# Kernel optimization log

Hardware: AMD Instinct MI355X
Metric: run time of the kernel (lower is better)

Reference implementation:

```python
import jax, jax.numpy as jnp
import numpy as np

B, N = 32, 1000
HID, COM = 256, 64
T_LEN, NOP = 288, 3
NVAL, TP_D, CS_D, TIME_D = 9, 2, 4, 4
IN_C = CS_D + TP_D + NVAL            # 15, competition GAT input
IN_CO = IN_C + COM                    # 79, cooperation GAT input
OBS = TIME_D + TP_D + CS_D + 2 * COM + NVAL  # 147
K_D = K_F = 500                       # int(0.5*N + 0.5)
TEMP = 1.0
NEG = jnp.float32(-1e8)


def setup_inputs() -> dict:
    key = jax.random.key(0)
    ks = jax.random.split(key, 24)
    def nrm(k, shp, scale=0.05):
        return (jax.random.normal(k, shp, dtype=jnp.float32) * scale)
    return {
        "time_idx": jax.random.randint(ks[0], (B, N), 0, T_LEN, dtype=jnp.int32),
        "op_idx": jax.random.randint(ks[1], (B, N), 0, NOP, dtype=jnp.int32),
        "value_feats": jax.random.normal(ks[2], (B, N, NVAL), dtype=jnp.float32),
        "dpcs_mark": jax.random.randint(ks[3], (B, N, 1), 0, 2) > 0,
        "adj_comp": jax.random.randint(ks[4], (B, N, N), 0, 2) > 0,
        "adj_coop": jax.random.randint(ks[5], (B, N, N), 0, 2) > 0,
        "distance": jax.random.uniform(ks[6], (N, N), dtype=jnp.float32),
        "time_tab": jax.random.uniform(ks[7], (T_LEN, TIME_D), dtype=jnp.float32),
        "tp_tab": jax.random.uniform(ks[8], (NOP, TP_D), dtype=jnp.float32),
        "cs_tab": jax.random.uniform(ks[9], (N, CS_D), dtype=jnp.float32),
        "Wc": nrm(ks[10], (IN_C, COM)),
        "asrc_c": nrm(ks[11], (COM,)),
        "adst_c": nrm(ks[12], (COM,)),
        "wd_c": jnp.float32(0.1),
        "Wco": nrm(ks[13], (IN_CO, COM)),
        "asrc_co": nrm(ks[14], (COM,)),
        "adst_co": nrm(ks[15], (COM,)),
        "wd_co": jnp.float32(0.1),
        "Wp": nrm(ks[16], (OBS, HID)),
        "bp": jnp.zeros((HID,), dtype=jnp.float32),
        "vpd": nrm(ks[17], (HID,)),
        "vpf": nrm(ks[18], (HID,)),
    }


def gat(x, W, a_src, a_dst, w_d, adj, dist):
    """Single-head GAT over dense boolean adjacency. adj[b,j,i] True => edge j->i."""
    h = jnp.einsum("bnf,fd->bnd", x, W)                       # (B,N,D)
    e = (jnp.einsum("bid,d->bi", h, a_dst)[:, :, None]        # dst term
         + jnp.einsum("bjd,d->bj", h, a_src)[:, None, :]      # src term
         + w_d * dist.T[None])                                 # dist[j,i] edge feat
    e = jax.nn.leaky_relu(e, 0.2)
    mask = jnp.swapaxes(adj, 1, 2)                             # (B, dst i, src j)
    e = jnp.where(mask, e, NEG)
    alpha = jax.nn.softmax(e, axis=-1)
    alpha = jnp.where(mask, alpha, 0.0)                        # isolated nodes -> 0
    return jax.nn.elu(jnp.einsum("bij,bjd->bid", alpha, h))


def gated_pool(x_p, scores, valid, k, temp):
    scores = scores - scores.max(axis=1, keepdims=True)
    scores = jnp.where(valid, scores, NEG)                     # (B,N,1)
    val_topk = jax.lax.top_k(scores[..., 0], k)[0]             # (B,k)
    min_topk = val_topk.min(axis=-1)[:, None, None]
    scores = jnp.where(scores < min_topk, NEG, scores)
    w = jax.nn.softmax(scores / temp, axis=1)
    xg = x_p * w
    return jnp.concatenate([xg.sum(axis=1), xg.max(axis=1)], axis=-1)  # (B,2H)


def reference(time_idx, op_idx, value_feats, dpcs_mark, adj_comp, adj_coop,
              distance, time_tab, tp_tab, cs_tab, Wc, asrc_c, adst_c, wd_c,
              Wco, asrc_co, adst_co, wd_co, Wp, bp, vpd, vpf):
    time_e = time_tab[time_idx]                                # (B,N,4)
    tp_e = tp_tab[op_idx]                                      # (B,N,2)
    cs_e = jnp.broadcast_to(cs_tab[None], (B, N, CS_D))        # (B,N,4)
    vf_det = jax.lax.stop_gradient(value_feats)
    x = jnp.concatenate([cs_e, tp_e, vf_det], axis=-1)         # (B,N,15)
    comp_reps = gat(x, Wc, asrc_c, adst_c, wd_c, adj_comp, distance)
    x_m = jnp.concatenate([x, comp_reps], axis=-1)             # (B,N,79)
    coop_reps = gat(x_m, Wco, asrc_co, adst_co, wd_co, adj_coop, distance)
    sag = jnp.concatenate([time_e, cs_e, tp_e, value_feats, comp_reps, coop_reps], axis=-1)
    x_p = jnp.einsum("bnf,fh->bnh", sag, Wp) + bp              # (B,N,HID)
    scores_d = jnp.einsum("bnh,h->bn", x_p, vpd)[..., None]
    s_d = gated_pool(x_p, scores_d, dpcs_mark, K_D, TEMP)
    scores_f = jnp.einsum("bnh,h->bn", x_p, vpf)[..., None]
    s_f = gated_pool(x_p, scores_f, ~dpcs_mark, K_F, TEMP)
    return jnp.concatenate([s_f, s_d], axis=-1)                # (B, 4*HID)
```

## Files before the change

### kernel.cpp

```cpp
#include <hip/hip_runtime.h>
#include <hip/hip_bf16.h>

#define NB 32
#define NN 1000
#define COMD 64
#define HIDD 256
#define KSEL 500
#define TI 16
#define GATX ((NN + TI - 1) / TI)
#define PACKX 32
#define NSPL 32
#define ROWS 32
#define DSTRIDE 1024

#define PB_AQ1  0
#define PB_DT   1024
#define PB_WP   1280
#define PB_WCO  1320
#define PB_MISC 1344
#define PB_EMB  1345
#define PB_N    (PB_EMB + NB * NN / 4)

typedef __hip_bfloat16 bf16;
typedef unsigned long long u64;
typedef __attribute__((ext_vector_type(4))) float f32x4;
typedef __attribute__((ext_vector_type(8))) short s16x8;
typedef __attribute__((ext_vector_type(4))) short s16x4;
typedef __attribute__((ext_vector_type(4))) unsigned short u16x4;
typedef __attribute__((ext_vector_type(2))) unsigned long long u64x2;

__device__ __forceinline__ float b2f(bf16 x){ return __bfloat162float(x); }

template<bool F32>
__device__ __forceinline__ float ldf(const void* p, long i){
  return F32 ? ((const float*)p)[i] : b2f(((const bf16*)p)[i]);
}
template<bool BINT>
__device__ __forceinline__ bool ldb(const void* p, long i){
  return BINT ? (((const int*)p)[i] != 0) : (((const unsigned char*)p)[i] != 0);
}

__device__ __forceinline__ float wave_sum(float v){
#pragma unroll
  for (int o = 32; o > 0; o >>= 1) v += __shfl_down(v, o, 64);
  return v;
}
__device__ __forceinline__ float wave_bsum(float v){
#pragma unroll
  for (int o = 32; o > 0; o >>= 1) v += __shfl_xor(v, o, 64);
  return v;
}
__device__ __forceinline__ float wave_bmax(float v){
#pragma unroll
  for (int o = 32; o > 0; o >>= 1) v = fmaxf(v, __shfl_xor(v, o, 64));
  return v;
}
__device__ __forceinline__ int wave_bsum_i(int v){
#pragma unroll
  for (int o = 32; o > 0; o >>= 1) v += __shfl_xor(v, o, 64);
  return v;
}
__device__ __forceinline__ unsigned fkey(float f){
// ... 184 lines not shown
  }
  ad = wave_bsum(ad); af = wave_bsum(af);
  if (lane == 0){ wv_ws[f] = ad; wv_ws[160 + f] = af; }
}
template<bool F32>
__device__ __forceinline__ void wco_role(const void* Wco, const void* asrc, const void* adst,
                         short* WcoB_hi, short* WcoB_lo, float* pvco, int rel){
  int t = threadIdx.x;
  int g = t >> 6, lane = t & 63;
  int f = rel * 4 + g;
  float w = (f < 79) ? ldf<F32>(Wco, (long)f * COMD + lane) : 0.f;
  int kb = f >> 5, q = (f >> 3) & 3, u = f & 7;
  long off = (((long)(kb * 4 + q)) * 64 + lane) * 8 + u;
  short hi, lo; split_bf(w, hi, lo);
  WcoB_hi[off] = hi; WcoB_lo[off] = lo;
  float dd = wave_bsum(w * ldf<F32>(adst, lane));
  float ss = wave_bsum(w * ldf<F32>(asrc, lane));
  if (lane == 0){ pvco[f] = dd; pvco[96 + f] = ss; }
}
template<bool F32>
__device__ __forceinline__ void misc_role(const void* wdc, const void* wdco,
                          const void* bp, const void* vpd, const void* vpf,
                          int f32, int as_int,
                          int* flags, float* wd_ws, float* wv_ws){
  int t = threadIdx.x;
  if (t >= 64) return;
  int lane = t;
  float ad = 0.f, af = 0.f;
#pragma unroll
  for (int r = 0; r < 4; ++r){
    int ch = r * 64 + lane;
    float bb = ldf<F32>(bp, ch);
    ad += bb * ldf<F32>(vpd, ch);
    af += bb * ldf<F32>(vpf, ch);
  }
  ad = wave_bsum(ad); af = wave_bsum(af);
  if (lane == 0){
    wv_ws[320] = ad; wv_ws[321] = af;
    wd_ws[0] = ldf<F32>(wdc, 0);
    wd_ws[1] = ldf<F32>(wdco, 0);
    flags[0] = f32; flags[1] = as_int;
  }
}
template<bool F32>
__device__ __forceinline__ void embed_body(
    const int* op_idx, const void* vf, const void* cs_tab, const void* tp_tab,
    const void* Wc, const void* asrc, const void* adst,
    float* x_out, short* hB_hi, short* hB_lo, float* ed_out, float* es_out,
    int rel){
  int t = threadIdx.x;
// ... 7 lines not shown
    float x_f;
    if (f < 4)      x_f = ldf<F32>(cs_tab, n * 4 + f);
    else if (f < 6) x_f = ldf<F32>(tp_tab, op * 2 + (f - 4));
    else            x_f = ldf<F32>(vf, (long)g * 9 + (f - 6));
    if (lane == f) xv = x_f;
    hacc += x_f * ldf<F32>(Wc, f * COMD + lane);
  }
  if (lane < 15) x_out[g * 15 + lane] = xv;
  hB_write(hB_hi, hB_lo, b, n, lane, hacc);
  float sd = wave_sum(hacc * ldf<F32>(adst, lane));
  float ss = wave_sum(hacc * ldf<F32>(asrc, lane));
  if (lane == 0){ ed_out[g] = sd; es_out[g] = ss; }
}
__global__ void __launch_bounds__(256) k_prep(
    const void* dist, const void* adj_comp,
    const void* wdc, const void* wdco,
    const void* Wp, const void* vpd, const void* vpf, const void* bp,
    const void* Wco, const void* asrc_co, const void* adst_co,
    const int* op_idx, const void* vfeat, const void* cs_tab, const void* tp_tab,
    const void* Wc, const void* asrc_c, const void* adst_c,
    int* flags, float* wd_ws, bf16* distTb, u64* adjQc,
    short* WpB_hi, short* WpB_lo, float* wv_ws,
    short* WcoB_hi, short* WcoB_lo, float* pvco,
    float* x_ws, short* hB_hi, short* hB_lo, float* ed_c, float* es_c){
  __shared__ __attribute__((aligned(16))) char smem[SMEM_BYTES];
  int blk = blockIdx.x;
  int f32, as_int;
  sniff2(dist, adj_comp, threadIdx.x & 63, f32, as_int);
  if (blk < PB_DT){
    if (as_int) adjq_role<true >(adj_comp, adjQc, blk - PB_AQ1, smem);
    else        adjq_role<false>(adj_comp, adjQc, blk - PB_AQ1, smem);
  } else if (blk < PB_WP){
    if (f32) dist_t_role<true >(dist, distTb, blk - PB_DT, smem);
    else     dist_t_role<false>(dist, distTb, blk - PB_DT, smem);
  } else if (blk < PB_WCO){
    if (f32) wp_role<true >(Wp, vpd, vpf, WpB_hi, WpB_lo, wv_ws, blk - PB_WP);
    else     wp_role<false>(Wp, vpd, vpf, WpB_hi, WpB_lo, wv_ws, blk - PB_WP);
  } else if (blk < PB_MISC){
    if (f32) wco_role<true >(Wco, asrc_co, adst_co, WcoB_hi, WcoB_lo, pvco, blk - PB_WCO);
    else     wco_role<false>(Wco, asrc_co, adst_co, WcoB_hi, WcoB_lo, pvco, blk - PB_WCO);
  } else if (blk < PB_EMB){
    if (f32) misc_role<true >(wdc, wdco, bp, vpd, vpf, f32, as_int, flags, wd_ws, wv_ws);
    else     misc_role<false>(wdc, wdco, bp, vpd, vpf, f32, as_int, flags, wd_ws, wv_ws);
  } else {
    if (f32) embed_body<true >(op_idx, vfeat, cs_tab, tp_tab, Wc, asrc_c, adst_c,
                               x_ws, hB_hi, hB_lo, ed_c, es_c, blk - PB_EMB);
    else     embed_body<false>(op_idx, vfeat, cs_tab, tp_tab, Wc, asrc_c, adst_c,
                               x_ws, hB_hi, hB_lo, ed_c, es_c, blk - PB_EMB);
  }
}

template<bool HCO>
__device__ __forceinline__ void gat_body(
    const float* __restrict__ ed, const float* __restrict__ es,
    const float* __restrict__ wd_ws, int wd_idx, const u64* __restrict__ adjQ,
    const bf16* __restrict__ distTb,
    const short* __restrict__ hB_hi, const short* __restrict__ hB_lo,
    float* __restrict__ reps,
    const int* __restrict__ flags, const void* adj_raw, u64* adjQ_out,
    const float* __restrict__ x_ws,
    const short* __restrict__ WcoB_hi, const short* __restrict__ WcoB_lo,
    const float* __restrict__ pvco,
    short* hB2_hi, short* hB2_lo, float* ed_o, float* es_o){
  __shared__ short pA[32 * 544] __attribute__((aligned(16)));
  __shared__ float redz[TI][4];
  __shared__ float esred[4];
  if (HCO && blockIdx.x >= GATX){
    int rel = (blockIdx.x - GATX) * NB + blockIdx.y;
    if (flags[1]) adjq_role<true >(adj_raw, adjQ_out, rel, (void*)pA);
    else          adjq_role<false>(adj_raw, adjQ_out, rel, (void*)pA);
    return;
  }
  int t = threadIdx.x;
  int wv = t >> 6, lane = t & 63;
  int b = blockIdx.y;
  int i0 = blockIdx.x * TI;
  float wd = wd_ws[wd_idx];
  int iw = i0 >> 6;
  int sb2 = (i0 & 63) >> 2;
  int j0 = t * 4;

  const u64* aq = adjQ + ((long)b * 16 + iw) * 1024 + j0;
  u64x2 wA = *(const u64x2*)&aq[0];
  u64x2 wB = *(const u64x2*)&aq[2];
  u64 wsh[4] = { wA[0] >> sb2, wA[1] >> sb2, wB[0] >> sb2, wB[1] >> sb2 };
  float4 es4 = *(const float4*)&es[(long)b * NN + j0];
  float esv[4] = {es4.x, es4.y, es4.z, es4.w};
  float esm = -1e30f;
#pragma unroll
  for (int c = 0; c < 4; ++c)
// ... 51 lines not shown
  int q = lane >> 4, m = lane & 15;
  int abase = q * 136 + m * 8;
  int ch = wv * 16 + m;
  const short* bh = hB_hi + (long)b * 65536 + ((long)q * 64 + ch) * 8;
  const short* bl = hB_lo + (long)b * 65536 + ((long)q * 64 + ch) * 8;
  f32x4 acc = {0.f, 0.f, 0.f, 0.f};
#pragma unroll
  for (int kb = 0; kb < 32; ++kb){
    s16x8 a   = *(const s16x8*)&pA[kb * 544 + abase];
    s16x8 bhi = *(const s16x8*)&bh[(long)kb * 2048];
    s16x8 blo = *(const s16x8*)&bl[(long)kb * 2048];
    acc = __builtin_amdgcn_mfma_f32_16x16x32_bf16(a, bhi, acc, 0, 0, 0);
    acc = __builtin_amdgcn_mfma_f32_16x16x32_bf16(a, blo, acc, 0, 0, 0);
  }
  float vr[4];
#pragma unroll
  for (int reg = 0; reg < 4; ++reg){
    int ti = (lane >> 4) * 4 + reg;
    float z = redz[ti][0] + redz[ti][1] + redz[ti][2] + redz[ti][3];
    float zi = (z > 0.f) ? 1.f / z : 0.f;
    float v = acc[reg] * zi;
    v = (v > 0.f) ? v : expm1f(v);
    vr[reg] = v;
    int ch2 = wv * 16 + (lane & 15);
    if (i0 + ti < NN)
      reps[((long)b * NN + i0 + ti) * COMD + ch2] = v;
  }
  if (!HCO) return;

  __syncthreads();
  float* cx = (float*)pA;
  short* cA_hi = pA + 2560;
  short* cA_lo = pA + 2560 + 1920;
  {
    int ch2 = wv * 16 + (lane & 15);
#pragma unroll
    for (int reg = 0; reg < 4; ++reg){
      int row = (lane >> 4) * 4 + reg;
      cx[row * 80 + 15 + ch2] = vr[reg];
    }
  }
  for (int idx = t; idx < 16 * 15; idx += 256){
    int nl = idx / 15, f = idx - nl * 15;
    int i = i0 + nl; int ic = (i < NN) ? i : (NN - 1);
    cx[nl * 80 + f] = x_ws[((long)b * NN + ic) * 15 + f];
  }
  __syncthreads();
  {
    int node = t >> 4, sub = t & 15;
    float dd = 0.f, ss = 0.f;
    for (int f = sub; f < 79; f += 16){
      float c = cx[node * 80 + f];
      dd += c * pvco[f];
      ss += c * pvco[96 + f];
    }
#pragma unroll
    for (int o = 8; o > 0; o >>= 1){
      dd += __shfl_xor(dd, o, 64);
      ss += __shfl_xor(ss, o, 64);
    }
    if (sub == 0 && i0 + node < NN){
      ed_o[(long)b * NN + i0 + node] = dd;
      es_o[(long)b * NN + i0 + node] = ss;
    }
  }
  for (int idx = t; idx < 16 * 96; idx += 256){
    int mm = idx / 96, k = idx - mm * 96;
    float v = (k < 79) ? cx[mm * 80 + k] : 0.f;
    int kb = k >> 5, qq = (k >> 3) & 3, u = k & 7;
    short hi, lo; split_bf(v, hi, lo);
    int off = (kb * 16 + mm) * 40 + qq * 8 + u;
    cA_hi[off] = hi; cA_lo[off] = lo;
  }
  __syncthreads();
  {
    int q2 = lane >> 4, m2 = lane & 15;
    int ch3 = wv * 16 + m2;
    f32x4 a2 = {0.f, 0.f, 0.f, 0.f};
#pragma unroll
    for (int kb = 0; kb < 3; ++kb){
      int aoff = (kb * 16 + m2) * 40 + q2 * 8;
      s16x8 a_hi = *(const s16x8*)&cA_hi[aoff];
      s16x8 a_lo = *(const s16x8*)&cA_lo[aoff];
      long boff = (((long)(kb * 4 + q2)) * 64 + ch3) * 8;
      s16x8 b_hi = *(const s16x8*)&WcoB_hi[boff];
      s16x8 b_lo = *(const s16x8*)&WcoB_lo[boff];
      a2 = __builtin_amdgcn_mfma_f32_16x16x32_bf16(a_hi, b_hi, a2, 0, 0, 0);
      a2 = __builtin_amdgcn_mfma_f32_16x16x32_bf16(a_hi, b_lo, a2, 0, 0, 0);
      a2 = __builtin_amdgcn_mfma_f32_16x16x32_bf16(a_lo, b_hi, a2, 0, 0, 0);
    }
#pragma unroll
    for (int reg = 0; reg < 4; ++reg){
      int row = (lane >> 4) * 4 + reg;
      int n2 = i0 + row;
      hB_write(hB2_hi, hB2_lo, b, n2, ch3, a2[reg]);
    }
  }
}
__global__ void __launch_bounds__(256) k_gat1(
    const float* ed, const float* es, const float* wd_ws, const u64* adjQ,
    const bf16* distTb, const short* hB_hi, const short* hB_lo, float* reps,
    const int* flags, const void* adj_raw, u64* adjQ_out,
    const float* x_ws, const short* WcoB_hi, const short* WcoB_lo,
    const float* pvco, short* hB2_hi, short* hB2_lo, float* ed_o, float* es_o){
  gat_body<true>(ed, es, wd_ws, 0, adjQ, distTb, hB_hi, hB_lo, reps,
                 flags, adj_raw, adjQ_out, x_ws, WcoB_hi, WcoB_lo, pvco,
                 hB2_hi, hB2_lo, ed_o, es_o);
}
__global__ void __launch_bounds__(256) k_gat2(
    const float* ed, const float* es, const float* wd_ws, const u64* adjQ,
    const bf16* distTb, const short* hB_hi, const short* hB_lo, float* reps){
  gat_body<false>(ed, es, wd_ws, 1, adjQ, distTb, hB_hi, hB_lo, reps,
                  nullptr, nullptr, nullptr, nullptr, nullptr, nullptr,
                  nullptr, nullptr, nullptr, nullptr, nullptr);
}

template<bool F32>
__device__ __forceinline__ void xp_body(
    const int* time_idx, const int* op_idx, const void* vf, const void* time_tab,
    const void* cs_tab, const void* tp_tab, const float* comp, const float* coop,
    const short* __restrict__ WpB_hi, const short* __restrict__ WpB_lo,
    const float* __restrict__ wv_ws, const void* bp,
    float* x_p, float* scf, float* scd){
  __shared__ float sagF[16][148] __attribute__((aligned(16)));
  __shared__ short sagA_hi[5 * 16 * 40] __attribute__((aligned(16)));
  __shared__ short sagA_lo[5 * 16 * 40] __attribute__((aligned(16)));
  int t = threadIdx.x;
  int wv = t >> 6, lane = t & 63;
  int base = blockIdx.x * 16;

  for (int idx = t; idx < 16 * 147; idx += 256){
    int nl = idx / 147, f = idx - nl * 147;
    int g = base + nl;
    int n = g % NN;
    float v;
    if (f < 4)       v = ldf<F32>(time_tab, time_idx[g] * 4 + f);
    else if (f < 8)  v = ldf<F32>(cs_tab, n * 4 + (f - 4));
    else if (f < 10) v = ldf<F32>(tp_tab, op_idx[g] * 2 + (f - 8));
    else if (f < 19) v = ldf<F32>(vf, (long)g * 9 + (f - 10));
    else if (f < 83) v = comp[(long)g * COMD + (f - 19)];
    else             v = coop[(long)g * COMD + (f - 83)];
    sagF[nl][f] = v;
  }
  __syncthreads();

  for (int idx = t; idx < 16 * 160; idx += 256){
    int m = idx / 160, k = idx - m * 160;
    float v = (k < 147) ? sagF[m][k] : 0.f;
    int kb = k >> 5, q = (k >> 3) & 3, u = k & 7;
    short hi, lo; split_bf(v, hi, lo);
    int off = (kb * 16 + m) * 40 + q * 8 + u;
    sagA_hi[off] = hi; sagA_lo[off] = lo;
  }
  {
    int node = t >> 4, sub = t & 15;
    float ad = 0.f, af = 0.f;
    for (int f = sub; f < 147; f += 16){
      float s = sagF[node][f];
      ad += s * wv_ws[f];
      af += s * wv_ws[160 + f];
    }
#pragma unroll
    for (int o = 8; o > 0; o >>= 1){
      ad += __shfl_xor(ad, o, 64);
      af += __shfl_xor(af, o, 64);
    }
    if (sub == 0){
      scd[base + node] = ad + wv_ws[320];
      scf[base + node] = af + wv_ws[321];
    }
  }
  __syncthreads();

  int Ag = lane >> 4, Am = lane & 15;
  f32x4 acc[4] = {{0,0,0,0},{0,0,0,0},{0,0,0,0},{0,0,0,0}};
#pragma unroll
  for (int kb = 0; kb < 5; ++kb){
    int aoff = (kb * 16 + Am) * 40 + Ag * 8;
    s16x8 a_hi = *(const s16x8*)&sagA_hi[aoff];
    s16x8 a_lo = *(const s16x8*)&sagA_lo[aoff];
#pragma unroll
    for (int ct = 0; ct < 4; ++ct){
      int ch = wv * 64 + ct * 16 + Am;
      long boff = (((long)(kb * 4 + Ag)) * 256 + ch) * 8;
      s16x8 b_hi = *(const s16x8*)&WpB_hi[boff];
      s16x8 b_lo = *(const s16x8*)&WpB_lo[boff];
      acc[ct] = __builtin_amdgcn_mfma_f32_16x16x32_bf16(a_hi, b_hi, acc[ct], 0, 0, 0);
      acc[ct] = __builtin_amdgcn_mfma_f32_16x16x32_bf16(a_hi, b_lo, acc[ct], 0, 0, 0);
      acc[ct] = __builtin_amdgcn_mfma_f32_16x16x32_bf16(a_lo, b_hi, acc[ct], 0, 0, 0);
    }
  }
#pragma unroll
  for (int ct = 0; ct < 4; ++ct){
    int ch = wv * 64 + ct * 16 + (lane & 15);
    float bb = ldf<F32>(bp, ch);
#pragma unroll
    for (int reg = 0; reg < 4; ++reg){
      int row = (lane >> 4) * 4 + reg;
      x_p[(long)(base + row) * HIDD + ch] = acc[ct][reg] + bb;
    }
  }
}
__global__ void __launch_bounds__(256) k_xp(
    const int* flags, const int* time_idx, const int* op_idx, const void* vf,
    const void* time_tab, const void* cs_tab, const void* tp_tab,
    const float* comp, const float* coop,
    const short* WpB_hi, const short* WpB_lo, const float* wv_ws, const void* bp,
    float* x_p, float* scf, float* scd){
  if (flags[0]) xp_body<true >(time_idx, op_idx, vf, time_tab, cs_tab, tp_tab, comp, coop, WpB_hi, WpB_lo, wv_ws, bp, x_p, scf, scd);
  else          xp_body<false>(time_idx, op_idx, vf, time_tab, cs_tab, tp_tab, comp, coop, WpB_hi, WpB_lo, wv_ws, bp, x_p, scf, scd);
}

template<bool BINT>
__device__ __forceinline__ void topk_body(
    const float* scf, const float* scd, const void* mark, float* wls){
  int lane = threadIdx.x;
  int b = blockIdx.x, pool = blockIdx.y;
  const float* sc = (pool == 0) ? scf : scd;
  float v[16]; unsigned key[16];
  float m0 = -INFINITY;
#pragma unroll
  for (int r = 0; r < 16; ++r){
    int n = r * 64 + lane;
    float s = (n < NN) ? sc[b * NN + n] : -INFINITY;
    v[r] = s;
    m0 = fmaxf(m0, s);
  }
  m0 = wave_bmax(m0);
  float m1 = -INFINITY;
#pragma unroll
  for (int r = 0; r < 16; ++r){
    int n = r * 64 + lane;
    bool valid = false;
    if (n < NN){
      bool mk = ldb<BINT>(mark, b * NN + n);
      valid = (pool == 0) ? !mk : mk;
    }
    v[r] = valid ? (v[r] - m0) : -1e8f;
    key[r] = fkey(v[r]);
    if (n < NN) m1 = fmaxf(m1, v[r]);
  }
  m1 = wave_bmax(m1);

  unsigned lo = 0u, hi = 0xFFFFFFFFu;
  while (lo < hi){
    unsigned mid = lo + ((hi - lo) >> 1) + 1u;
    int c = 0;
#pragma unroll
    for (int r = 0; r < 16; ++r) c += (key[r] >= mid) ? 1 : 0;
    c = wave_bsum_i(c);
    if (c >= KSEL) lo = mid; else hi = mid - 1u;
  }

  float p[16];
  float ls = 0.f;
#pragma unroll
  for (int r = 0; r < 16; ++r){
    int n = r * 64 + lane;
    float pp = (n < NN && key[r] >= lo) ? __expf(v[r] - m1) : 0.f;
    p[r] = pp;
    ls += pp;
  }
  ls = wave_bsum(ls);
  float zinv = (ls > 0.f) ? 1.f / ls : 0.f;
  float* w_out = wls + ((long)b * 2 + pool) * 1024;
#pragma unroll
  for (int r = 0; r < 16; ++r){
    int n = r * 64 + lane;
    if (n < NN) w_out[n] = p[r] * zinv;
  }
}
__global__ void k_topk(const int* flags, const float* scf, const float* scd,
                       const void* mark, float* wls){
  if (flags[1]) topk_body<true >(scf, scd, mark, wls);
  else          topk_body<false>(scf, scd, mark, wls);
}

__global__ void __launch_bounds__(256) k_psum(
    const float* __restrict__ wls, const float* __restrict__ x_p,
    float* __restrict__ part){
  __shared__ float wf[ROWS], wdd[ROWS];
  int t = threadIdx.x;
  int b = blockIdx.x, z = blockIdx.y;
  int n0 = z * ROWS;
  int ns = min(ROWS, NN - n0);
  if (t < ns){
    wf[t]  = wls[((long)b * 2 + 0) * 1024 + n0 + t];
    wdd[t] = wls[((long)b * 2 + 1) * 1024 + n0 + t];
  }
  __syncthreads();
  float sf = 0.f, mf = -INFINITY, sd = 0.f, md = -INFINITY;
  const float* xb = x_p + ((long)b * NN + n0) * HIDD + t;
  for (int k = 0; k < ns; ++k){
    float xv = xb[(long)k * HIDD];
    float gf = wf[k] * xv;
    float gd = wdd[k] * xv;
    sf += gf; mf = fmaxf(mf, gf);
    sd += gd; md = fmaxf(md, gd);
  }
  long pb = (((long)b * NSPL + z) * 4) * HIDD + t;
  part[pb + 0 * HIDD] = sf;
  part[pb + 1 * HIDD] = mf;
  part[pb + 2 * HIDD] = sd;
  part[pb + 3 * HIDD] = md;
}

template<bool F32>
__device__ __forceinline__ void pfin_body(const float* part, void* out){
  int t = threadIdx.x;
  int b = blockIdx.x;
  float sf = 0.f, mf = -INFINITY, sd = 0.f, md = -INFINITY;
#pragma unroll
  for (int z = 0; z < NSPL; ++z){
    long pb = (((long)b * NSPL + z) * 4) * HIDD + t;
    sf += part[pb + 0 * HIDD];
    mf = fmaxf(mf, part[pb + 1 * HIDD]);
    sd += part[pb + 2 * HIDD];
    md = fmaxf(md, part[pb + 3 * HIDD]);
  }
  long ob = (long)b * 1024;
  if (F32){
    ((float*)out)[ob + t] = sf;
    ((float*)out)[ob + 256 + t] = mf;
    ((float*)out)[ob + 512 + t] = sd;
    ((float*)out)[ob + 768 + t] = md;
  } else {
    ((bf16*)out)[ob + t] = __float2bfloat16(sf);
    ((bf16*)out)[ob + 256 + t] = __float2bfloat16(mf);
    ((bf16*)out)[ob + 512 + t] = __float2bfloat16(sd);
    ((bf16*)out)[ob + 768 + t] = __float2bfloat16(md);
  }
}
__global__ void k_pfin(const int* flags, const float* part, void* out){
  if (flags[0]) pfin_body<true >(part, out);
  else          pfin_body<false>(part, out);
}

extern "C" void kernel_launch(void* const* d_in, const int* in_sizes, int n_in,
                              void* d_out, int out_size, void* d_ws, size_t ws_size,
                              hipStream_t stream){
  const int*  time_idx = (const int*)d_in[0];
  const int*  op_idx   = (const int*)d_in[1];
  const void* vfeat    = d_in[2];
  const void* dpcs     = d_in[3];
  const void* adj_comp = d_in[4];
  const void* adj_coop = d_in[5];
  const void* dist     = d_in[6];
  const void* time_tab = d_in[7];
  const void* tp_tab   = d_in[8];
  const void* cs_tab   = d_in[9];
  const void* Wc       = d_in[10];
  const void* asrc_c   = d_in[11];
  const void* adst_c   = d_in[12];
  const void* wd_c     = d_in[13];
  const void* Wco      = d_in[14];
  const void* asrc_co  = d_in[15];
  const void* adst_co  = d_in[16];
  const void* wd_co    = d_in[17];
  const void* Wp       = d_in[18];
  const void* bp       = d_in[19];
  const void* vpd      = d_in[20];
  const void* vpf      = d_in[21];

  char* ws = (char*)d_ws;
  size_t o = 0;
  auto alloc = [&](size_t bytes)->char*{
    char* p = ws + o; o = (o + bytes + 255) & ~(size_t)255; return p;
  };
  int*   flags   = (int*)alloc(16);
  float* wd_ws   = (float*)alloc(8);
  bf16*  distTb  = (bf16*)alloc((size_t)NN * DSTRIDE * 2);
  u64*   adjQc   = (u64*)alloc((size_t)NB * 16 * 1024 * 8);
  u64*   adjQo   = (u64*)alloc((size_t)NB * 16 * 1024 * 8);
  float* x_ws    = (float*)alloc((size_t)NB * NN * 15 * 4);
  float* comp    = (float*)alloc((size_t)NB * NN * COMD * 4);
  float* coop    = (float*)alloc((size_t)NB * NN * COMD * 4);
  short* hB_hi   = (short*)alloc((size_t)NB * 65536 * 2);
  short* hB_lo   = (short*)alloc((size_t)NB * 65536 * 2);
  short* hB2_hi  = (short*)alloc((size_t)NB * 65536 * 2);
  short* hB2_lo  = (short*)alloc((size_t)NB * 65536 * 2);
  short* WpB_hi  = (short*)alloc((size_t)5 * 4 * 256 * 8 * 2);
  short* WpB_lo  = (short*)alloc((size_t)5 * 4 * 256 * 8 * 2);
  short* WcoB_hi = (short*)alloc((size_t)3 * 4 * 64 * 8 * 2);
  short* WcoB_lo = (short*)alloc((size_t)3 * 4 * 64 * 8 * 2);
  float* wv_ws   = (float*)alloc(322 * 4);
  float* pvco    = (float*)alloc(192 * 4);
  float* ed_c    = (float*)alloc((size_t)NB * NN * 4 + 256);
  float* es_c    = (float*)alloc((size_t)NB * NN * 4 + 256);
  float* ed_o    = (float*)alloc((size_t)NB * NN * 4 + 256);
  float* es_o    = (float*)alloc((size_t)NB * NN * 4 + 256);
  float* scf     = (float*)alloc((size_t)NB * NN * 4);
  float* scd     = (float*)alloc((size_t)NB * NN * 4);
  float* wls     = (float*)alloc((size_t)NB * 2 * 1024 * 4);
  float* part    = (float*)alloc((size_t)NB * NSPL * 4 * HIDD * 4);
  float* x_p     = (float*)alloc((size_t)NB * NN * HIDD * 4);

  k_prep<<<dim3(PB_N), dim3(256), 0, stream>>>(
      dist, adj_comp, wd_c, wd_co, Wp, vpd, vpf, bp,
      Wco, asrc_co, adst_co,
      op_idx, vfeat, cs_tab, tp_tab, Wc, asrc_c, adst_c,
      flags, wd_ws, distTb, adjQc, WpB_hi, WpB_lo, wv_ws,
      WcoB_hi, WcoB_lo, pvco,
      x_ws, hB_hi, hB_lo, ed_c, es_c);
  k_gat1<<<dim3(GATX + PACKX, NB), dim3(256), 0, stream>>>(
      ed_c, es_c, wd_ws, adjQc, distTb, hB_hi, hB_lo, comp,
      flags, adj_coop, adjQo,
      x_ws, WcoB_hi, WcoB_lo, pvco, hB2_hi, hB2_lo, ed_o, es_o);
  k_gat2<<<dim3(GATX, NB), dim3(256), 0, stream>>>(
      ed_o, es_o, wd_ws, adjQo, distTb, hB2_hi, hB2_lo, coop);
  k_xp<<<dim3(NB * NN / 16), dim3(256), 0, stream>>>(
      flags, time_idx, op_idx, vfeat, time_tab, cs_tab, tp_tab, comp, coop,
      WpB_hi, WpB_lo, wv_ws, bp, x_p, scf, scd);
  k_topk<<<dim3(NB, 2), dim3(64), 0, stream>>>(flags, scf, scd, dpcs, wls);
  k_psum<<<dim3(NB, NSPL), dim3(256), 0, stream>>>(wls, x_p, part);
  k_pfin<<<dim3(NB), dim3(256), 0, stream>>>(flags, part, d_out);
}
```

Baseline: 465.7 us.

## Fuse projection into second GAT and merge topk/psum/finalize into one pool kernel

The x_p projection (sag concat plus the Wp MFMA) now runs inside the second GAT kernel's epilogue, so coop reps are never written to or re-read from global memory. Top-k selection, the weighted partial sums and the final reduction are merged into one pool kernel that uses an atomic counter so the last block per batch finalizes. This removes three kernel launches and the coop and wls round trips. In exchange, every pool block recomputes the top-k threshold redundantly, and the counter reset depends on the prep kernel.

```diff
diff --git a/kernel.cpp b/kernel.cpp
--- a/kernel.cpp
+++ b/kernel.cpp
@@ -35,9 +35,8 @@
 __device__ __forceinline__ float ldf(const void* p, long i){
   return F32 ? ((const float*)p)[i] : b2f(((const bf16*)p)[i]);
 }
-template<bool BINT>
-__device__ __forceinline__ bool ldb(const void* p, long i){
-  return BINT ? (((const int*)p)[i] != 0) : (((const unsigned char*)p)[i] != 0);
+__device__ __forceinline__ float ldr(const void* p, long i, int f32){
+  return f32 ? ((const float*)p)[i] : b2f(((const bf16*)p)[i]);
 }
 
 __device__ __forceinline__ float wave_sum(float v){
@@ -268,10 +267,11 @@
 __device__ __forceinline__ void misc_role(const void* wdc, const void* wdco,
                           const void* bp, const void* vpd, const void* vpf,
                           int f32, int as_int,
-                          int* flags, float* wd_ws, float* wv_ws){
+                          int* flags, float* wd_ws, float* wv_ws, int* ctr){
   int t = threadIdx.x;
   if (t >= 64) return;
   int lane = t;
+  if (lane < NB) ctr[lane] = 0;
   float ad = 0.f, af = 0.f;
 #pragma unroll
   for (int r = 0; r < 4; ++r){
@@ -325,7 +325,8 @@
     int* flags, float* wd_ws, bf16* distTb, u64* adjQc,
     short* WpB_hi, short* WpB_lo, float* wv_ws,
     short* WcoB_hi, short* WcoB_lo, float* pvco,
-    float* x_ws, short* hB_hi, short* hB_lo, float* ed_c, float* es_c){
+    float* x_ws, short* hB_hi, short* hB_lo, float* ed_c, float* es_c,
+    int* ctr){
   __shared__ __attribute__((aligned(16))) char smem[SMEM_BYTES];
   int blk = blockIdx.x;
   int f32, as_int;
@@ -343,8 +344,8 @@
     if (f32) wco_role<true >(Wco, asrc_co, adst_co, WcoB_hi, WcoB_lo, pvco, blk - PB_WCO);
     else     wco_role<false>(Wco, asrc_co, adst_co, WcoB_hi, WcoB_lo, pvco, blk - PB_WCO);
   } else if (blk < PB_EMB){
-    if (f32) misc_role<true >(wdc, wdco, bp, vpd, vpf, f32, as_int, flags, wd_ws, wv_ws);
-    else     misc_role<false>(wdc, wdco, bp, vpd, vpf, f32, as_int, flags, wd_ws, wv_ws);
+    if (f32) misc_role<true >(wdc, wdco, bp, vpd, vpf, f32, as_int, flags, wd_ws, wv_ws, ctr);
+    else     misc_role<false>(wdc, wdco, bp, vpd, vpf, f32, as_int, flags, wd_ws, wv_ws, ctr);
   } else {
     if (f32) embed_body<true >(op_idx, vfeat, cs_tab, tp_tab, Wc, asrc_c, adst_c,
                                x_ws, hB_hi, hB_lo, ed_c, es_c, blk - PB_EMB);
@@ -353,7 +354,7 @@
   }
 }
 
-template<bool HCO>
+template<int MODE>
 __device__ __forceinline__ void gat_body(
     const float* __restrict__ ed, const float* __restrict__ es,
     const float* __restrict__ wd_ws, int wd_idx, const u64* __restrict__ adjQ,
@@ -364,11 +365,17 @@
     const float* __restrict__ x_ws,
     const short* __restrict__ WcoB_hi, const short* __restrict__ WcoB_lo,
     const float* __restrict__ pvco,
-    short* hB2_hi, short* hB2_lo, float* ed_o, float* es_o){
+    short* hB2_hi, short* hB2_lo, float* ed_o, float* es_o,
+    const int* __restrict__ time_idx, const int* __restrict__ op_idx,
+    const void* vf, const void* time_tab, const void* cs_tab, const void* tp_tab,
+    const float* __restrict__ comp,
+    const short* __restrict__ WpB_hi, const short* __restrict__ WpB_lo,
+    const float* __restrict__ wv_ws, const void* bp,
+    float* x_p, float* scf_o, float* scd_o){
   __shared__ short pA[32 * 544] __attribute__((aligned(16)));
   __shared__ float redz[TI][4];
   __shared__ float esred[4];
-  if (HCO && blockIdx.x >= GATX){
+  if (MODE == 0 && blockIdx.x >= GATX){
     int rel = (blockIdx.x - GATX) * NB + blockIdx.y;
     if (flags[1]) adjq_role<true >(adj_raw, adjQ_out, rel, (void*)pA);
     else          adjq_role<false>(adj_raw, adjQ_out, rel, (void*)pA);
@@ -466,78 +473,164 @@
     float v = acc[reg] * zi;
     v = (v > 0.f) ? v : expm1f(v);
     vr[reg] = v;
-    int ch2 = wv * 16 + (lane & 15);
-    if (i0 + ti < NN)
-      reps[((long)b * NN + i0 + ti) * COMD + ch2] = v;
-  }
-  if (!HCO) return;
-
-  __syncthreads();
-  float* cx = (float*)pA;
-  short* cA_hi = pA + 2560;
-  short* cA_lo = pA + 2560 + 1920;
-  {
-    int ch2 = wv * 16 + (lane & 15);
-#pragma unroll
-    for (int reg = 0; reg < 4; ++reg){
-      int row = (lane >> 4) * 4 + reg;
-      cx[row * 80 + 15 + ch2] = vr[reg];
-    }
-  }
-  for (int idx = t; idx < 16 * 15; idx += 256){
-    int nl = idx / 15, f = idx - nl * 15;
-    int i = i0 + nl; int ic = (i < NN) ? i : (NN - 1);
-    cx[nl * 80 + f] = x_ws[((long)b * NN + ic) * 15 + f];
-  }
-  __syncthreads();
-  {
-    int node = t >> 4, sub = t & 15;
-    float dd = 0.f, ss = 0.f;
-    for (int f = sub; f < 79; f += 16){
-      float c = cx[node * 80 + f];
-      dd += c * pvco[f];
-      ss += c * pvco[96 + f];
-    }
-#pragma unroll
-    for (int o = 8; o > 0; o >>= 1){
-      dd += __shfl_xor(dd, o, 64);
-      ss += __shfl_xor(ss, o, 64);
-    }
-    if (sub == 0 && i0 + node < NN){
-      ed_o[(long)b * NN + i0 + node] = dd;
-      es_o[(long)b * NN + i0 + node] = ss;
-    }
-  }
-  for (int idx = t; idx < 16 * 96; idx += 256){
-    int mm = idx / 96, k = idx - mm * 96;
-    float v = (k < 79) ? cx[mm * 80 + k] : 0.f;
-    int kb = k >> 5, qq = (k >> 3) & 3, u = k & 7;
-    short hi, lo; split_bf(v, hi, lo);
-    int off = (kb * 16 + mm) * 40 + qq * 8 + u;
-    cA_hi[off] = hi; cA_lo[off] = lo;
-  }
-  __syncthreads();
-  {
-    int q2 = lane >> 4, m2 = lane & 15;
-    int ch3 = wv * 16 + m2;
-    f32x4 a2 = {0.f, 0.f, 0.f, 0.f};
-#pragma unroll
-    for (int kb = 0; kb < 3; ++kb){
-      int aoff = (kb * 16 + m2) * 40 + q2 * 8;
-      s16x8 a_hi = *(const s16x8*)&cA_hi[aoff];
-      s16x8 a_lo = *(const s16x8*)&cA_lo[aoff];
-      long boff = (((long)(kb * 4 + q2)) * 64 + ch3) * 8;
-      s16x8 b_hi = *(const s16x8*)&WcoB_hi[boff];
-      s16x8 b_lo = *(const s16x8*)&WcoB_lo[boff];
-      a2 = __builtin_amdgcn_mfma_f32_16x16x32_bf16(a_hi, b_hi, a2, 0, 0, 0);
-      a2 = __builtin_amdgcn_mfma_f32_16x16x32_bf16(a_hi, b_lo, a2, 0, 0, 0);
-      a2 = __builtin_amdgcn_mfma_f32_16x16x32_bf16(a_lo, b_hi, a2, 0, 0, 0);
-    }
-#pragma unroll
-    for (int reg = 0; reg < 4; ++reg){
-      int row = (lane >> 4) * 4 + reg;
-      int n2 = i0 + row;
-      hB_write(hB2_hi, hB2_lo, b, n2, ch3, a2[reg]);
+    if (MODE == 0){
+      int ch2 = wv * 16 + (lane & 15);
+      if (i0 + ti < NN)
+        reps[((long)b * NN + i0 + ti) * COMD + ch2] = v;
+    }
+  }
+
+  if (MODE == 0){
+    __syncthreads();
+    float* cx = (float*)pA;
+    short* cA_hi = pA + 2560;
+    short* cA_lo = pA + 2560 + 1920;
+    {
+      int ch2 = wv * 16 + (lane & 15);
+#pragma unroll
+      for (int reg = 0; reg < 4; ++reg){
+        int row = (lane >> 4) * 4 + reg;
+        cx[row * 80 + 15 + ch2] = vr[reg];
+      }
+    }
+    for (int idx = t; idx < 16 * 15; idx += 256){
+      int nl = idx / 15, f = idx - nl * 15;
+      int i = i0 + nl; int ic = (i < NN) ? i : (NN - 1);
+      cx[nl * 80 + f] = x_ws[((long)b * NN + ic) * 15 + f];
+    }
+    __syncthreads();
+    {
+      int node = t >> 4, sub = t & 15;
+      float dd = 0.f, ss = 0.f;
+      for (int f = sub; f < 79; f += 16){
+        float c = cx[node * 80 + f];
+        dd += c * pvco[f];
+        ss += c * pvco[96 + f];
+      }
+#pragma unroll
+      for (int o = 8; o > 0; o >>= 1){
+        dd += __shfl_xor(dd, o, 64);
+        ss += __shfl_xor(ss, o, 64);
+      }
+      if (sub == 0 && i0 + node < NN){
+        ed_o[(long)b * NN + i0 + node] = dd;
+        es_o[(long)b * NN + i0 + node] = ss;
+      }
+    }
+    for (int idx = t; idx < 16 * 96; idx += 256){
+      int mm = idx / 96, k = idx - mm * 96;
+      float v = (k < 79) ? cx[mm * 80 + k] : 0.f;
+      int kb = k >> 5, qq = (k >> 3) & 3, u = k & 7;
+      short hi, lo; split_bf(v, hi, lo);
+      int off = (kb * 16 + mm) * 40 + qq * 8 + u;
+      cA_hi[off] = hi; cA_lo[off] = lo;
+    }
+    __syncthreads();
+    {
+      int q2 = lane >> 4, m2 = lane & 15;
+      int ch3 = wv * 16 + m2;
+      f32x4 a2 = {0.f, 0.f, 0.f, 0.f};
+#pragma unroll
+      for (int kb = 0; kb < 3; ++kb){
+        int aoff = (kb * 16 + m2) * 40 + q2 * 8;
+        s16x8 a_hi = *(const s16x8*)&cA_hi[aoff];
+        s16x8 a_lo = *(const s16x8*)&cA_lo[aoff];
+        long boff = (((long)(kb * 4 + q2)) * 64 + ch3) * 8;
+        s16x8 b_hi = *(const s16x8*)&WcoB_hi[boff];
+        s16x8 b_lo = *(const s16x8*)&WcoB_lo[boff];
+        a2 = __builtin_amdgcn_mfma_f32_16x16x32_bf16(a_hi, b_hi, a2, 0, 0, 0);
+        a2 = __builtin_amdgcn_mfma_f32_16x16x32_bf16(a_hi, b_lo, a2, 0, 0, 0);
+        a2 = __builtin_amdgcn_mfma_f32_16x16x32_bf16(a_lo, b_hi, a2, 0, 0, 0);
+      }
+#pragma unroll
+      for (int reg = 0; reg < 4; ++reg){
+        int row = (lane >> 4) * 4 + reg;
+        int n2 = i0 + row;
+        hB_write(hB2_hi, hB2_lo, b, n2, ch3, a2[reg]);
+      }
+    }
+  } else {
+    __syncthreads();
+    float* sagF = (float*)pA;
+    short* sgA_hi = pA + 4736;
+    short* sgA_lo = pA + 7936;
+    int f32 = flags[0];
+    {
+      int ch2 = wv * 16 + (lane & 15);
+#pragma unroll
+      for (int reg = 0; reg < 4; ++reg){
+        int row = (lane >> 4) * 4 + reg;
+        sagF[row * 148 + 83 + ch2] = vr[reg];
+      }
+    }
+    for (int idx = t; idx < 16 * 83; idx += 256){
+      int nl = idx / 83, f = idx - nl * 83;
+      int n = i0 + nl; int ic = (n < NN) ? n : (NN - 1);
+      long g = (long)b * NN + ic;
+      float v;
+      if (f < 4)       v = ldr(time_tab, (long)time_idx[g] * 4 + f, f32);
+      else if (f < 8)  v = ldr(cs_tab, ic * 4 + (f - 4), f32);
+      else if (f < 10) v = ldr(tp_tab, (long)op_idx[g] * 2 + (f - 8), f32);
+      else if (f < 19) v = ldr(vf, g * 9 + (f - 10), f32);
+      else             v = comp[g * COMD + (f - 19)];
+      sagF[nl * 148 + f] = v;
+    }
+    __syncthreads();
+    for (int idx = t; idx < 16 * 160; idx += 256){
+      int mm = idx / 160, k = idx - mm * 160;
+      float v = (k < 147) ? sagF[mm * 148 + k] : 0.f;
+      int kb = k >> 5, qq = (k >> 3) & 3, u = k & 7;
+      short hi, lo; split_bf(v, hi, lo);
+      int off = (kb * 16 + mm) * 40 + qq * 8 + u;
+      sgA_hi[off] = hi; sgA_lo[off] = lo;
+    }
+    {
+      int node = t >> 4, sub = t & 15;
+      float ad = 0.f, af = 0.f;
+      for (int f = sub; f < 147; f += 16){
+        float s = sagF[node * 148 + f];
+        ad += s * wv_ws[f];
+        af += s * wv_ws[160 + f];
+      }
+#pragma unroll
+      for (int o = 8; o > 0; o >>= 1){
+        ad += __shfl_xor(ad, o, 64);
+        af += __shfl_xor(af, o, 64);
+      }
+      if (sub == 0 && i0 + node < NN){
+        scd_o[(long)b * NN + i0 + node] = ad + wv_ws[320];
+        scf_o[(long)b * NN + i0 + node] = af + wv_ws[321];
+      }
+    }
+    __syncthreads();
+    int Ag = lane >> 4, Am = lane & 15;
+    f32x4 acc2[4] = {{0,0,0,0},{0,0,0,0},{0,0,0,0},{0,0,0,0}};
+#pragma unroll
+    for (int kb = 0; kb < 5; ++kb){
+      int aoff = (kb * 16 + Am) * 40 + Ag * 8;
+      s16x8 a_hi = *(const s16x8*)&sgA_hi[aoff];
+      s16x8 a_lo = *(const s16x8*)&sgA_lo[aoff];
+#pragma unroll
+      for (int ct = 0; ct < 4; ++ct){
+        int ch3 = wv * 64 + ct * 16 + Am;
+        long boff = (((long)(kb * 4 + Ag)) * 256 + ch3) * 8;
+        s16x8 b_hi = *(const s16x8*)&WpB_hi[boff];
+        s16x8 b_lo = *(const s16x8*)&WpB_lo[boff];
+        acc2[ct] = __builtin_amdgcn_mfma_f32_16x16x32_bf16(a_hi, b_hi, acc2[ct], 0, 0, 0);
+        acc2[ct] = __builtin_amdgcn_mfma_f32_16x16x32_bf16(a_hi, b_lo, acc2[ct], 0, 0, 0);
+        acc2[ct] = __builtin_amdgcn_mfma_f32_16x16x32_bf16(a_lo, b_hi, acc2[ct], 0, 0, 0);
+      }
+    }
+#pragma unroll
+    for (int ct = 0; ct < 4; ++ct){
+      int ch3 = wv * 64 + ct * 16 + (lane & 15);
+      float bb = ldr(bp, ch3, f32);
+#pragma unroll
+      for (int reg = 0; reg < 4; ++reg){
+        int row = (lane >> 4) * 4 + reg;
+        if (i0 + row < NN)
+          x_p[((long)b * NN + i0 + row) * HIDD + ch3] = acc2[ct][reg] + bb;
+      }
     }
   }
 }
@@ -547,192 +640,95 @@
     const int* flags, const void* adj_raw, u64* adjQ_out,
     const float* x_ws, const short* WcoB_hi, const short* WcoB_lo,
     const float* pvco, short* hB2_hi, short* hB2_lo, float* ed_o, float* es_o){
-  gat_body<true>(ed, es, wd_ws, 0, adjQ, distTb, hB_hi, hB_lo, reps,
-                 flags, adj_raw, adjQ_out, x_ws, WcoB_hi, WcoB_lo, pvco,
-                 hB2_hi, hB2_lo, ed_o, es_o);
-}
-__global__ void __launch_bounds__(256) k_gat2(
+  gat_body<0>(ed, es, wd_ws, 0, adjQ, distTb, hB_hi, hB_lo, reps,
+              flags, adj_raw, adjQ_out, x_ws, WcoB_hi, WcoB_lo, pvco,
+              hB2_hi, hB2_lo, ed_o, es_o,
+              nullptr, nullptr, nullptr, nullptr, nullptr, nullptr,
+              nullptr, nullptr, nullptr, nullptr, nullptr,
+              nullptr, nullptr, nullptr);
+}
+__global__ void __launch_bounds__(256) k_gat2x(
     const float* ed, const float* es, const float* wd_ws, const u64* adjQ,
-    const bf16* distTb, const short* hB_hi, const short* hB_lo, float* reps){
-  gat_body<false>(ed, es, wd_ws, 1, adjQ, distTb, hB_hi, hB_lo, reps,
-                  nullptr, nullptr, nullptr, nullptr, nullptr, nullptr,
-                  nullptr, nullptr, nullptr, nullptr, nullptr);
-}
-
-template<bool F32>
-__device__ __forceinline__ void xp_body(
-    const int* time_idx, const int* op_idx, const void* vf, const void* time_tab,
-    const void* cs_tab, const void* tp_tab, const float* comp, const float* coop,
-    const short* __restrict__ WpB_hi, const short* __restrict__ WpB_lo,
-    const float* __restrict__ wv_ws, const void* bp,
+    const bf16* distTb, const short* hB_hi, const short* hB_lo,
+    const int* flags,
+    const int* time_idx, const int* op_idx, const void* vf,
+    const void* time_tab, const void* cs_tab, const void* tp_tab,
+    const float* comp, const short* WpB_hi, const short* WpB_lo,
+    const float* wv_ws, const void* bp,
     float* x_p, float* scf, float* scd){
-  __shared__ float sagF[16][148] __attribute__((aligned(16)));
-  __shared__ short sagA_hi[5 * 16 * 40] __attribute__((aligned(16)));
-  __shared__ short sagA_lo[5 * 16 * 40] __attribute__((aligned(16)));
+  gat_body<1>(ed, es, wd_ws, 1, adjQ, distTb, hB_hi, hB_lo, nullptr,
+              flags, nullptr, nullptr, nullptr, nullptr, nullptr, nullptr,
+              nullptr, nullptr, nullptr, nullptr,
+              time_idx, op_idx, vf, time_tab, cs_tab, tp_tab,
+              comp, WpB_hi, WpB_lo, wv_ws, bp, x_p, scf, scd);
+}
+
+__global__ void __launch_bounds__(256) k_pool(
+    const int* __restrict__ flags, const float* __restrict__ scf,
+    const float* __restrict__ scd, const void* __restrict__ mark,
+    const float* __restrict__ x_p, float* __restrict__ part,
+    int* __restrict__ ctr, void* __restrict__ out){
+  __shared__ float wf[ROWS], wdd[ROWS];
+  __shared__ int lastf;
   int t = threadIdx.x;
   int wv = t >> 6, lane = t & 63;
-  int base = blockIdx.x * 16;
-
-  for (int idx = t; idx < 16 * 147; idx += 256){
-    int nl = idx / 147, f = idx - nl * 147;
-    int g = base + nl;
-    int n = g % NN;
-    float v;
-    if (f < 4)       v = ldf<F32>(time_tab, time_idx[g] * 4 + f);
-    else if (f < 8)  v = ldf<F32>(cs_tab, n * 4 + (f - 4));
-    else if (f < 10) v = ldf<F32>(tp_tab, op_idx[g] * 2 + (f - 8));
-    else if (f < 19) v = ldf<F32>(vf, (long)g * 9 + (f - 10));
-    else if (f < 83) v = comp[(long)g * COMD + (f - 19)];
-    else             v = coop[(long)g * COMD + (f - 83)];
-    sagF[nl][f] = v;
-  }
-  __syncthreads();
-
-  for (int idx = t; idx < 16 * 160; idx += 256){
-    int m = idx / 160, k = idx - m * 160;
-    float v = (k < 147) ? sagF[m][k] : 0.f;
-    int kb = k >> 5, q = (k >> 3) & 3, u = k & 7;
-    short hi, lo; split_bf(v, hi, lo);
-    int off = (kb * 16 + m) * 40 + q * 8 + u;
-    sagA_hi[off] = hi; sagA_lo[off] = lo;
-  }
-  {
-    int node = t >> 4, sub = t & 15;
-    float ad = 0.f, af = 0.f;
-    for (int f = sub; f < 147; f += 16){
-      float s = sagF[node][f];
-      ad += s * wv_ws[f];
-      af += s * wv_ws[160 + f];
-    }
-#pragma unroll
-    for (int o = 8; o > 0; o >>= 1){
-      ad += __shfl_xor(ad, o, 64);
-      af += __shfl_xor(af, o, 64);
-    }
-    if (sub == 0){
-      scd[base + node] = ad + wv_ws[320];
-      scf[base + node] = af + wv_ws[321];
-    }
-  }
-  __syncthreads();
-
-  int Ag = lane >> 4, Am = lane & 15;
-  f32x4 acc[4] = {{0,0,0,0},{0,0,0,0},{0,0,0,0},{0,0,0,0}};
-#pragma unroll
-  for (int kb = 0; kb < 5; ++kb){
-    int aoff = (kb * 16 + Am) * 40 + Ag * 8;
-    s16x8 a_hi = *(const s16x8*)&sagA_hi[aoff];
-    s16x8 a_lo = *(const s16x8*)&sagA_lo[aoff];
-#pragma unroll
-    for (int ct = 0; ct < 4; ++ct){
-      int ch = wv * 64 + ct * 16 + Am;
-      long boff = (((long)(kb * 4 + Ag)) * 256 + ch) * 8;
-      s16x8 b_hi = *(const s16x8*)&WpB_hi[boff];
-      s16x8 b_lo = *(const s16x8*)&WpB_lo[boff];
-      acc[ct] = __builtin_amdgcn_mfma_f32_16x16x32_bf16(a_hi, b_hi, acc[ct], 0, 0, 0);
-      acc[ct] = __builtin_amdgcn_mfma_f32_16x16x32_bf16(a_hi, b_lo, acc[ct], 0, 0, 0);
-      acc[ct] = __builtin_amdgcn_mfma_f32_16x16x32_bf16(a_lo, b_hi, acc[ct], 0, 0, 0);
-    }
-  }
-#pragma unroll
-  for (int ct = 0; ct < 4; ++ct){
-    int ch = wv * 64 + ct * 16 + (lane & 15);
-    float bb = ldf<F32>(bp, ch);
-#pragma unroll
-    for (int reg = 0; reg < 4; ++reg){
-      int row = (lane >> 4) * 4 + reg;
-      x_p[(long)(base + row) * HIDD + ch] = acc[ct][reg] + bb;
-    }
-  }
-}
-__global__ void __launch_bounds__(256) k_xp(
-    const int* flags, const int* time_idx, const int* op_idx, const void* vf,
-    const void* time_tab, const void* cs_tab, const void* tp_tab,
-    const float* comp, const float* coop,
-    const short* WpB_hi, const short* WpB_lo, const float* wv_ws, const void* bp,
-    float* x_p, float* scf, float* scd){
-  if (flags[0]) xp_body<true >(time_idx, op_idx, vf, time_tab, cs_tab, tp_tab, comp, coop, WpB_hi, WpB_lo, wv_ws, bp, x_p, scf, scd);
-  else          xp_body<false>(time_idx, op_idx, vf, time_tab, cs_tab, tp_tab, comp, coop, WpB_hi, WpB_lo, wv_ws, bp, x_p, scf, scd);
-}
-
-template<bool BINT>
-__device__ __forceinline__ void topk_body(
-    const float* scf, const float* scd, const void* mark, float* wls){
-  int lane = threadIdx.x;
-  int b = blockIdx.x, pool = blockIdx.y;
-  const float* sc = (pool == 0) ? scf : scd;
-  float v[16]; unsigned key[16];
-  float m0 = -INFINITY;
-#pragma unroll
-  for (int r = 0; r < 16; ++r){
-    int n = r * 64 + lane;
-    float s = (n < NN) ? sc[b * NN + n] : -INFINITY;
-    v[r] = s;
-    m0 = fmaxf(m0, s);
-  }
-  m0 = wave_bmax(m0);
-  float m1 = -INFINITY;
-#pragma unroll
-  for (int r = 0; r < 16; ++r){
-    int n = r * 64 + lane;
-    bool valid = false;
-    if (n < NN){
-      bool mk = ldb<BINT>(mark, b * NN + n);
-      valid = (pool == 0) ? !mk : mk;
-    }
-    v[r] = valid ? (v[r] - m0) : -1e8f;
-    key[r] = fkey(v[r]);
-    if (n < NN) m1 = fmaxf(m1, v[r]);
-  }
-  m1 = wave_bmax(m1);
-
-  unsigned lo = 0u, hi = 0xFFFFFFFFu;
-  while (lo < hi){
-    unsigned mid = lo + ((hi - lo) >> 1) + 1u;
-    int c = 0;
-#pragma unroll
-    for (int r = 0; r < 16; ++r) c += (key[r] >= mid) ? 1 : 0;
-    c = wave_bsum_i(c);
-    if (c >= KSEL) lo = mid; else hi = mid - 1u;
-  }
-
-  float p[16];
-  float ls = 0.f;
-#pragma unroll
-  for (int r = 0; r < 16; ++r){
-    int n = r * 64 + lane;
-    float pp = (n < NN && key[r] >= lo) ? __expf(v[r] - m1) : 0.f;
-    p[r] = pp;
-    ls += pp;
-  }
-  ls = wave_bsum(ls);
-  float zinv = (ls > 0.f) ? 1.f / ls : 0.f;
-  float* w_out = wls + ((long)b * 2 + pool) * 1024;
-#pragma unroll
-  for (int r = 0; r < 16; ++r){
-    int n = r * 64 + lane;
-    if (n < NN) w_out[n] = p[r] * zinv;
-  }
-}
-__global__ void k_topk(const int* flags, const float* scf, const float* scd,
-                       const void* mark, float* wls){
-  if (flags[1]) topk_body<true >(scf, scd, mark, wls);
-  else          topk_body<false>(scf, scd, mark, wls);
-}
-
-__global__ void __launch_bounds__(256) k_psum(
-    const float* __restrict__ wls, const float* __restrict__ x_p,
-    float* __restrict__ part){
-  __shared__ float wf[ROWS], wdd[ROWS];
-  int t = threadIdx.x;
   int b = blockIdx.x, z = blockIdx.y;
   int n0 = z * ROWS;
+  int f32 = flags[0], bint = flags[1];
+  if (wv < 2){
+    int pool = wv;
+    const float* sc = pool ? scd : scf;
+    float v[16]; unsigned key[16];
+    float m0 = -INFINITY;
+#pragma unroll
+    for (int r = 0; r < 16; ++r){
+      int n = r * 64 + lane;
+      float s = (n < NN) ? sc[b * NN + n] : -INFINITY;
+      v[r] = s; m0 = fmaxf(m0, s);
+    }
+    m0 = wave_bmax(m0);
+    float m1 = -INFINITY;
+#pragma unroll
+    for (int r = 0; r < 16; ++r){
+      int n = r * 64 + lane;
+      bool valid = false;
+      if (n < NN){
+        bool mk = bint ? (((const int*)mark)[b * NN + n] != 0)
+                       : (((const unsigned char*)mark)[b * NN + n] != 0);
+        valid = (pool == 0) ? !mk : mk;
+      }
+      v[r] = valid ? (v[r] - m0) : -1e8f;
+      key[r] = fkey(v[r]);
+      if (n < NN) m1 = fmaxf(m1, v[r]);
+    }
+    m1 = wave_bmax(m1);
+    unsigned lo = 0u, hi = 0xFFFFFFFFu;
+    while (lo < hi){
+      unsigned mid = lo + ((hi - lo) >> 1) + 1u;
+      int c = 0;
+#pragma unroll
+      for (int r = 0; r < 16; ++r) c += (key[r] >= mid) ? 1 : 0;
+      c = wave_bsum_i(c);
+      if (c >= KSEL) lo = mid; else hi = mid - 1u;
+    }
+    float ls = 0.f; float p[16];
+#pragma unroll
+    for (int r = 0; r < 16; ++r){
+      int n = r * 64 + lane;
+      float pp = (n < NN && key[r] >= lo) ? __expf(v[r] - m1) : 0.f;
+      p[r] = pp; ls += pp;
+    }
+    ls = wave_bsum(ls);
+    float zinv = (ls > 0.f) ? 1.f / ls : 0.f;
+    float* wdst = pool ? wdd : wf;
+#pragma unroll
+    for (int r = 0; r < 16; ++r){
+      int n = r * 64 + lane;
+      if (n >= n0 && n < n0 + ROWS && n < NN) wdst[n - n0] = p[r] * zinv;
+    }
+  }
+  __syncthreads();
   int ns = min(ROWS, NN - n0);
-  if (t < ns){
-    wf[t]  = wls[((long)b * 2 + 0) * 1024 + n0 + t];
-    wdd[t] = wls[((long)b * 2 + 1) * 1024 + n0 + t];
-  }
-  __syncthreads();
   float sf = 0.f, mf = -INFINITY, sd = 0.f, md = -INFINITY;
   const float* xb = x_p + ((long)b * NN + n0) * HIDD + t;
   for (int k = 0; k < ns; ++k){
@@ -747,37 +743,31 @@
   part[pb + 1 * HIDD] = mf;
   part[pb + 2 * HIDD] = sd;
   part[pb + 3 * HIDD] = md;
-}
-
-template<bool F32>
-__device__ __forceinline__ void pfin_body(const float* part, void* out){
-  int t = threadIdx.x;
-  int b = blockIdx.x;
-  float sf = 0.f, mf = -INFINITY, sd = 0.f, md = -INFINITY;
-#pragma unroll
-  for (int z = 0; z < NSPL; ++z){
-    long pb = (((long)b * NSPL + z) * 4) * HIDD + t;
-    sf += part[pb + 0 * HIDD];
-    mf = fmaxf(mf, part[pb + 1 * HIDD]);
-    sd += part[pb + 2 * HIDD];
-    md = fmaxf(md, part[pb + 3 * HIDD]);
+  __threadfence();
+  if (t == 0) lastf = (atomicAdd(&ctr[b], 1) == NSPL - 1);
+  __syncthreads();
+  if (!lastf) return;
+  __threadfence();
+  float asf = 0.f, amf = -INFINITY, asd = 0.f, amd = -INFINITY;
+  for (int zz = 0; zz < NSPL; ++zz){
+    long qb = (((long)b * NSPL + zz) * 4) * HIDD + t;
+    asf += part[qb + 0 * HIDD];
+    amf = fmaxf(amf, part[qb + 1 * HIDD]);
+    asd += part[qb + 2 * HIDD];
+    amd = fmaxf(amd, part[qb + 3 * HIDD]);
   }
   long ob = (long)b * 1024;
-  if (F32){
-    ((float*)out)[ob + t] = sf;
-    ((float*)out)[ob + 256 + t] = mf;
-    ((float*)out)[ob + 512 + t] = sd;
-    ((float*)out)[ob + 768 + t] = md;
+  if (f32){
+    ((float*)out)[ob + t] = asf;
+    ((float*)out)[ob + 256 + t] = amf;
+    ((float*)out)[ob + 512 + t] = asd;
+    ((float*)out)[ob + 768 + t] = amd;
   } else {
-    ((bf16*)out)[ob + t] = __float2bfloat16(sf);
-    ((bf16*)out)[ob + 256 + t] = __float2bfloat16(mf);
-    ((bf16*)out)[ob + 512 + t] = __float2bfloat16(sd);
-    ((bf16*)out)[ob + 768 + t] = __float2bfloat16(md);
-  }
-}
-__global__ void k_pfin(const int* flags, const float* part, void* out){
-  if (flags[0]) pfin_body<true >(part, out);
-  else          pfin_body<false>(part, out);
+    ((bf16*)out)[ob + t] = __float2bfloat16(asf);
+    ((bf16*)out)[ob + 256 + t] = __float2bfloat16(amf);
+    ((bf16*)out)[ob + 512 + t] = __float2bfloat16(asd);
+    ((bf16*)out)[ob + 768 + t] = __float2bfloat16(amd);
+  }
 }
 
 extern "C" void kernel_launch(void* const* d_in, const int* in_sizes, int n_in,
@@ -813,12 +803,12 @@
   };
   int*   flags   = (int*)alloc(16);
   float* wd_ws   = (float*)alloc(8);
+  int*   ctr     = (int*)alloc(NB * 4);
   bf16*  distTb  = (bf16*)alloc((size_t)NN * DSTRIDE * 2);
   u64*   adjQc   = (u64*)alloc((size_t)NB * 16 * 1024 * 8);
   u64*   adjQo   = (u64*)alloc((size_t)NB * 16 * 1024 * 8);
   float* x_ws    = (float*)alloc((size_t)NB * NN * 15 * 4);
   float* comp    = (float*)alloc((size_t)NB * NN * COMD * 4);
-  float* coop    = (float*)alloc((size_t)NB * NN * COMD * 4);
   short* hB_hi   = (short*)alloc((size_t)NB * 65536 * 2);
   short* hB_lo   = (short*)alloc((size_t)NB * 65536 * 2);
   short* hB2_hi  = (short*)alloc((size_t)NB * 65536 * 2);
@@ -835,7 +825,6 @@
   float* es_o    = (float*)alloc((size_t)NB * NN * 4 + 256);
   float* scf     = (float*)alloc((size_t)NB * NN * 4);
   float* scd     = (float*)alloc((size_t)NB * NN * 4);
-  float* wls     = (float*)alloc((size_t)NB * 2 * 1024 * 4);
   float* part    = (float*)alloc((size_t)NB * NSPL * 4 * HIDD * 4);
   float* x_p     = (float*)alloc((size_t)NB * NN * HIDD * 4);
 
@@ -845,17 +834,15 @@
       op_idx, vfeat, cs_tab, tp_tab, Wc, asrc_c, adst_c,
       flags, wd_ws, distTb, adjQc, WpB_hi, WpB_lo, wv_ws,
       WcoB_hi, WcoB_lo, pvco,
-      x_ws, hB_hi, hB_lo, ed_c, es_c);
+      x_ws, hB_hi, hB_lo, ed_c, es_c, ctr);
   k_gat1<<<dim3(GATX + PACKX, NB), dim3(256), 0, stream>>>(
       ed_c, es_c, wd_ws, adjQc, distTb, hB_hi, hB_lo, comp,
       flags, adj_coop, adjQo,
       x_ws, WcoB_hi, WcoB_lo, pvco, hB2_hi, hB2_lo, ed_o, es_o);
-  k_gat2<<<dim3(GATX, NB), dim3(256), 0, stream>>>(
-      ed_o, es_o, wd_ws, adjQo, distTb, hB2_hi, hB2_lo, coop);
-  k_xp<<<dim3(NB * NN / 16), dim3(256), 0, stream>>>(
-      flags, time_idx, op_idx, vfeat, time_tab, cs_tab, tp_tab, comp, coop,
-      WpB_hi, WpB_lo, wv_ws, bp, x_p, scf, scd);
-  k_topk<<<dim3(NB, 2), dim3(64), 0, stream>>>(flags, scf, scd, dpcs, wls);
-  k_psum<<<dim3(NB, NSPL), dim3(256), 0, stream>>>(wls, x_p, part);
-  k_pfin<<<dim3(NB), dim3(256), 0, stream>>>(flags, part, d_out);
-}
+  k_gat2x<<<dim3(GATX, NB), dim3(256), 0, stream>>>(
+      ed_o, es_o, wd_ws, adjQo, distTb, hB2_hi, hB2_lo,
+      flags, time_idx, op_idx, vfeat, time_tab, cs_tab, tp_tab,
+      comp, WpB_hi, WpB_lo, wv_ws, bp, x_p, scf, scd);
+  k_pool<<<dim3(NB, NSPL), dim3(256), 0, stream>>>(
+      flags, scf, scd, dpcs, x_p, part, ctr, d_out);
+}
```

Result: slower. 543.1 us (+16.6%).
